# Optimization experiments

Measured on AMD Instinct MI355X. Metric: run time of the kernel, lower is better.

Reference implementation:

```python
import jax, jax.numpy as jnp
import numpy as np

# Offsets from init_kwargs: short- and long-range affinities along x and y.
OFFSETS = ((-1, 0), (0, -1), (-2, 0), (0, -2), (-4, 0), (0, -4), (-8, 0), (0, -8))
B, C, H, W = 1, 1, 4096, 4096
N_LABELS = 64


def setup_inputs() -> dict:
    key = jax.random.key(0)
    # Integer instance labels stored as float (module runs conv on float dtype).
    seg = jax.random.randint(key, (B, C, H, W), 0, N_LABELS).astype(jnp.float32)
    return {"segmentation": seg}


def _shift(x, ox, oy):
    """Zero-padded shift: out[i,j] = x[i+ox, j+oy] (0 outside).

    Exactly reproduces F.conv2d with the 3x3 kernel (-1 at center, +1 at the
    sign-determined corner), dilation=max(1,|off|), padding=max(1,|off|):
    the conv output equals shift(x, ox, oy) - x.
    """
    ax, ay = abs(ox), abs(oy)
    p = jnp.pad(x, ((0, 0), (0, 0), (ax, ax), (ay, ay)))
    Hh, Ww = x.shape[-2], x.shape[-1]
    return p[:, :, ax + ox:ax + ox + Hh, ay + oy:ay + oy + Ww]


def reference(segmentation) -> jnp.ndarray:
    seg = segmentation  # [B,1,H,W]
    affs = []
    for ox, oy in OFFSETS:  # small fixed offset list -> static unroll
        grad = _shift(seg, ox, oy) - seg          # spatial gradient
        aff = jnp.where(grad == 0, jnp.ones_like(grad), jnp.zeros_like(grad))
        affs.append(aff)
    out = jnp.stack(affs, axis=0)  # [O, B, 1, H, W]
    # torch .squeeze(1).squeeze(1) with B=1 -> [O, H, W]
    return out[:, 0, 0]
```

## Files before the change

### kernel.cpp

```cpp
#include <hip/hip_runtime.h>
#include <hip/hip_bf16.h>


#define IMG_H 4096
#define IMG_W 4096
#define BAND  16

typedef float floatx4 __attribute__((ext_vector_type(4)));

__device__ __forceinline__ float4 ld4(const float* p) { return *(const float4*)p; }

__device__ __forceinline__ void st4_nt(float* p, float4 v) {
    floatx4 x = { v.x, v.y, v.z, v.w };
    __builtin_nontemporal_store(x, (floatx4*)p);
}

__device__ __forceinline__ float4 eq4(float4 a, float4 b) {
    return make_float4(a.x == b.x ? 1.0f : 0.0f,
                       a.y == b.y ? 1.0f : 0.0f,
                       a.z == b.z ? 1.0f : 0.0f,
                       a.w == b.w ? 1.0f : 0.0f);
}

__global__ __launch_bounds__(256) void GetAffs_83416854823610_kernel(
        const float* __restrict__ seg, float* __restrict__ out) {
    const int jq = blockIdx.x * 256 + threadIdx.x;
    const int j  = jq << 2;
    const int i0 = blockIdx.y * BAND;
    const float4 zero4 = make_float4(0.f, 0.f, 0.f, 0.f);

    float4 hist[8];
#pragma unroll
    for (int k = 0; k < 8; ++k) {
        const int r = i0 - 8 + k;
        hist[k] = (r >= 0) ? ld4(seg + (size_t)r * IMG_W + j) : zero4;
    }

    const size_t HW = (size_t)IMG_H * IMG_W;

#pragma unroll
    for (int u = 0; u < BAND; ++u) {
        const int i = i0 + u;
        const float* row = seg + (size_t)i * IMG_W;
        const float4 c  = ld4(row + j);
        const float4 l1 = (j >= 4) ? ld4(row + j - 4) : zero4;
        const float4 l2 = (j >= 8) ? ld4(row + j - 8) : zero4;

        const float4 v1 = hist[(u + 7) & 7];
        const float4 v2 = hist[(u + 6) & 7];
        const float4 v4 = hist[(u + 4) & 7];
        const float4 v8 = hist[u & 7];

        const float4 h1 = make_float4(l1.w, c.x, c.y, c.z);
        const float4 h2 = make_float4(l1.z, l1.w, c.x, c.y);
        const float4 h4 = l1;
        const float4 h8 = l2;

        const size_t base = (size_t)i * IMG_W + (size_t)j;
        st4_nt(out + 0 * HW + base, eq4(v1, c));
        st4_nt(out + 1 * HW + base, eq4(h1, c));
        st4_nt(out + 2 * HW + base, eq4(v2, c));
        st4_nt(out + 3 * HW + base, eq4(h2, c));
        st4_nt(out + 4 * HW + base, eq4(v4, c));
        st4_nt(out + 5 * HW + base, eq4(h4, c));
        st4_nt(out + 6 * HW + base, eq4(v8, c));
        st4_nt(out + 7 * HW + base, eq4(h8, c));

        hist[u & 7] = c;
    }
}

extern "C" void kernel_launch(void* const* d_in, const int* in_sizes, int n_in,
                              void* d_out, int out_size, void* d_ws, size_t ws_size,
                              hipStream_t stream) {
    const float* seg = (const float*)d_in[0];
    float* out = (float*)d_out;
    dim3 grid((IMG_W / 4) / 256, IMG_H / BAND);
    dim3 block(256);
    GetAffs_83416854823610_kernel<<<grid, block, 0, stream>>>(seg, out);
}
```

Before: 575.4 us.

## Reorder stores plane-by-plane with full-row 1024-thread blocks and smaller bands

Each block now covers a full image row width with 1024 threads and an 8-row band. All rows are loaded into registers up front, and the output stores are regrouped so each affinity plane is written as a contiguous run of rows. The aim is write locality per output plane and fewer, larger blocks. The cost is more halo re-reads, since the 8 history rows are loaded per 8-row band, and higher register pressure under launch bounds of 1024 threads.

```diff
diff --git a/kernel.cpp b/kernel.cpp
--- a/kernel.cpp
+++ b/kernel.cpp
@@ -4,7 +4,7 @@
 
 #define IMG_H 4096
 #define IMG_W 4096
-#define BAND  16
+#define BAND  8
 
 typedef float floatx4 __attribute__((ext_vector_type(4)));
 
@@ -22,52 +22,46 @@
                        a.w == b.w ? 1.0f : 0.0f);
 }
 
-__global__ __launch_bounds__(256) void GetAffs_83416854823610_kernel(
+__global__ __launch_bounds__(1024, 4) void GetAffs_83416854823610_kernel(
         const float* __restrict__ seg, float* __restrict__ out) {
-    const int jq = blockIdx.x * 256 + threadIdx.x;
-    const int j  = jq << 2;
-    const int i0 = blockIdx.y * BAND;
+    const int j  = threadIdx.x << 2;
+    const int i0 = blockIdx.x * BAND;
     const float4 zero4 = make_float4(0.f, 0.f, 0.f, 0.f);
+    const size_t HW = (size_t)IMG_H * IMG_W;
 
-    float4 hist[8];
+    float4 c[16];
+
 #pragma unroll
-    for (int k = 0; k < 8; ++k) {
+    for (int k = 0; k < 16; ++k) {
         const int r = i0 - 8 + k;
-        hist[k] = (r >= 0) ? ld4(seg + (size_t)r * IMG_W + j) : zero4;
+        c[k] = (r >= 0) ? ld4(seg + (size_t)r * IMG_W + j) : zero4;
+        if (k >= 8) {
+            const float* row = seg + (size_t)r * IMG_W;
+            const float4 cc = c[k];
+            const float4 l1 = (j >= 4) ? ld4(row + j - 4) : zero4;
+            const float4 l2 = (j >= 8) ? ld4(row + j - 8) : zero4;
+            const float4 h1 = make_float4(l1.w, cc.x, cc.y, cc.z);
+            const float4 h2 = make_float4(l1.z, l1.w, cc.x, cc.y);
+            const size_t base = (size_t)r * IMG_W + (size_t)j;
+            st4_nt(out + 1 * HW + base, eq4(h1, cc));
+            st4_nt(out + 3 * HW + base, eq4(h2, cc));
+            st4_nt(out + 5 * HW + base, eq4(l1, cc));
+            st4_nt(out + 7 * HW + base, eq4(l2, cc));
+        }
     }
 
-    const size_t HW = (size_t)IMG_H * IMG_W;
+#define VPLANE(P, D)                                                        \
+    _Pragma("unroll")                                                       \
+    for (int u = 0; u < BAND; ++u) {                                        \
+        const size_t base = (size_t)(i0 + u) * IMG_W + (size_t)j;           \
+        st4_nt(out + (P) * HW + base, eq4(c[8 + u - (D)], c[8 + u]));       \
+    }
 
-#pragma unroll
-    for (int u = 0; u < BAND; ++u) {
-        const int i = i0 + u;
-        const float* row = seg + (size_t)i * IMG_W;
-        const float4 c  = ld4(row + j);
-        const float4 l1 = (j >= 4) ? ld4(row + j - 4) : zero4;
-        const float4 l2 = (j >= 8) ? ld4(row + j - 8) : zero4;
-
-        const float4 v1 = hist[(u + 7) & 7];
-        const float4 v2 = hist[(u + 6) & 7];
-        const float4 v4 = hist[(u + 4) & 7];
-        const float4 v8 = hist[u & 7];
-
-        const float4 h1 = make_float4(l1.w, c.x, c.y, c.z);
-        const float4 h2 = make_float4(l1.z, l1.w, c.x, c.y);
-        const float4 h4 = l1;
-        const float4 h8 = l2;
-
-        const size_t base = (size_t)i * IMG_W + (size_t)j;
-        st4_nt(out + 0 * HW + base, eq4(v1, c));
-        st4_nt(out + 1 * HW + base, eq4(h1, c));
-        st4_nt(out + 2 * HW + base, eq4(v2, c));
-        st4_nt(out + 3 * HW + base, eq4(h2, c));
-        st4_nt(out + 4 * HW + base, eq4(v4, c));
-        st4_nt(out + 5 * HW + base, eq4(h4, c));
-        st4_nt(out + 6 * HW + base, eq4(v8, c));
-        st4_nt(out + 7 * HW + base, eq4(h8, c));
-
-        hist[u & 7] = c;
-    }
+    VPLANE(0, 1)
+    VPLANE(2, 2)
+    VPLANE(4, 4)
+    VPLANE(6, 8)
+#undef VPLANE
 }
 
 extern "C" void kernel_launch(void* const* d_in, const int* in_sizes, int n_in,
@@ -75,7 +69,7 @@
                               hipStream_t stream) {
     const float* seg = (const float*)d_in[0];
     float* out = (float*)d_out;
-    dim3 grid((IMG_W / 4) / 256, IMG_H / BAND);
-    dim3 block(256);
+    dim3 grid(IMG_H / BAND);
+    dim3 block(1024);
     GetAffs_83416854823610_kernel<<<grid, block, 0, stream>>>(seg, out);
 }
```

Result: no change. 567.4 us (-1.4%).
